# Performance work log

Measured on AMD Instinct MI355X. Metric: run time of the kernel, lower is better.

## Reference

```python
import jax, jax.numpy as jnp
import numpy as np

N_TYPES = 10000   # len(fs.inodes)
HID = 256         # fs.size
BATCH = 32
SEQ = 1024


def _build_tree(rng):
    # random recursive tree: parent[i] uniform in [0, i), root parent = -1
    parent = np.full(N_TYPES, -1, np.int64)
    parent[1:] = (rng.random(N_TYPES - 1) * np.arange(1, N_TYPES)).astype(np.int64)
    # depth (number of nodes on root path incl. self)
    depth = np.ones(N_TYPES, np.int64)
    for i in range(1, N_TYPES):
        depth[i] = depth[parent[i]] + 1
    D = int(depth.max())
    # ancestor table: anc[n, d] = d-th ancestor of n (anc[n,0]=n), -1 padding
    anc = np.full((N_TYPES, D), -1, np.int32)
    anc[:, 0] = np.arange(N_TYPES)
    cur = parent.copy()
    for d in range(1, D):
        anc[:, d] = cur
        cur = np.where(cur >= 0, parent[np.maximum(cur, 0)], -1)
    return anc


def setup_inputs() -> dict:
    key = jax.random.key(0)
    ks = jax.random.split(key, 8)
    rng = np.random.default_rng(0)
    anc = jnp.asarray(_build_tree(rng))  # [N, D] int32
    k = 1.0 / np.sqrt(HID)
    inp = {
        "event_seqs": jax.random.randint(ks[0], (BATCH, SEQ), 0, N_TYPES),
        "anc": anc,
        "weight": jax.random.uniform(ks[1], (N_TYPES,), jnp.float32, -0.1, 0.1),
        "emb": jax.random.normal(ks[2], (N_TYPES, HID), jnp.float32),
        "W_ih": jax.random.uniform(ks[3], (4 * HID, HID), jnp.float32, -k, k),
        "W_hh": jax.random.uniform(ks[4], (4 * HID, HID), jnp.float32, -k, k),
        "b_ih": jax.random.uniform(ks[5], (4 * HID,), jnp.float32, -k, k),
        "b_hh": jax.random.uniform(ks[6], (4 * HID,), jnp.float32, -k, k),
    }
    return inp


def _path_table(anc, weight, emb):
    # path[n] = sum_d (prod_{j<d} weight[anc[n,j]]) * emb[anc[n,d]], over valid ancestors
    valid = anc >= 0                                  # [N, D]
    anc_safe = jnp.where(valid, anc, 0)
    w = jnp.where(valid, weight[anc_safe], 1.0)       # [N, D]
    cumw = jnp.cumprod(w, axis=1)
    cumw = jnp.concatenate([jnp.ones_like(cumw[:, :1]), cumw[:, :-1]], axis=1)
    cumw = jnp.where(valid, cumw, 0.0)
    e = emb[anc_safe]                                 # [N, D, H]
    return jnp.einsum("nd,ndh->nh", cumw, e)          # [N, H]


def _lstm(emb_seq, W_ih, W_hh, b_ih, b_hh):
    # emb_seq: [T, B, H]; torch LSTM gate order i, f, g, o
    H = W_hh.shape[1]
    B = emb_seq.shape[1]
    x_proj = jnp.einsum("tbh,gh->tbg", emb_seq, W_ih) + b_ih + b_hh  # [T, B, 4H]

    def step(carry, x_t):
        h, c = carry
        gates = x_t + h @ W_hh.T
        i, f, g, o = jnp.split(gates, 4, axis=-1)
        i, f, o = jax.nn.sigmoid(i), jax.nn.sigmoid(f), jax.nn.sigmoid(o)
        g = jnp.tanh(g)
        c = f * c + i * g
        h = o * jnp.tanh(c)
        return (h, c), h

    h0 = jnp.zeros((B, H), emb_seq.dtype)
    (hn, cn), out = jax.lax.scan(step, (h0, h0), x_proj)
    return out, hn, cn


def reference(event_seqs, anc, weight, emb, W_ih, W_hh, b_ih, b_hh):
    path = _path_table(anc, weight, emb)       # [N, H]
    emb_seq = path[event_seqs.T]               # [T, B, H] (torch transposes to seq-first)
    out, hn, cn = _lstm(emb_seq, W_ih, W_hh, b_ih, b_hh)
    return out
```

## Files before the change

kernel.cpp:

```cpp
#include <hip/hip_runtime.h>

typedef unsigned int uint;
typedef unsigned long long u64;
typedef _Float16 f16;
typedef _Float16 f16x2 __attribute__((ext_vector_type(2)));
typedef _Float16 f16x8 __attribute__((ext_vector_type(8)));
typedef float f32x4 __attribute__((ext_vector_type(4)));

#define N_TYPES 10000
#define HID 256
#define G4 1024
#define BATCH 32
#define SEQ 1024

__global__ void k_path(const int* __restrict__ anc, const float* __restrict__ weight,
                       const float* __restrict__ emb, int D, f16* __restrict__ path) {
  int n = blockIdx.x;
  int h = threadIdx.x;
  float acc = 0.f, cw = 1.f;
  for (int d = 0; d < D; ++d) {
    int a = anc[n * D + d];
    if (a < 0) break;
    acc += cw * emb[a * HID + h];
    cw *= weight[a];
  }
  path[n * HID + h] = (f16)acc;
}

__global__ void k_conv(const float* __restrict__ wih, const float* __restrict__ whh,
                       const float* __restrict__ bih, const float* __restrict__ bhh,
                       f16* __restrict__ wih_h, uint* __restrict__ whh_t,
                       float* __restrict__ bias) {
  int i = blockIdx.x * 256 + threadIdx.x;
  wih_h[i] = (f16)wih[i];
  if (i < G4 * 128) {
    int row = i >> 7, p = i & 127;
    f16x2 v;
    v.x = (f16)whh[row * HID + 2 * p];
    v.y = (f16)whh[row * HID + 2 * p + 1];
    whh_t[p * G4 + row] = __builtin_bit_cast(uint, v);
  }
  if (i < G4) bias[i] = bih[i] + bhh[i];
}

#define BM 128
#define BN 128
#define BK 64
#define LPAD 72
__global__ __launch_bounds__(256) void k_gemm(const f16* __restrict__ A,
                                              const f16* __restrict__ Bw,
                                              const float* __restrict__ bias,
                                              f16* __restrict__ C) {
  __shared__ f16 sA[BM][LPAD];
  __shared__ f16 sB[BN][LPAD];
  int m0 = blockIdx.x * BM, n0 = blockIdx.y * BN;
  int tid = threadIdx.x;
  int wid = tid >> 6, lane = tid & 63;
  int wm = wid & 1, wn = wid >> 1;
  f32x4 acc[4][4] = {};
  for (int k0 = 0; k0 < 256; k0 += BK) {
    __syncthreads();
    int r = tid >> 3, kc = (tid & 7) * 8;
    for (int i = 0; i < 4; ++i) {
      int row = r + 32 * i;
      int gm = m0 + row;
      uint4 va = make_uint4(0u, 0u, 0u, 0u);
      if (gm < N_TYPES) va = *(const uint4*)&A[gm * 256 + k0 + kc];
      *(uint4*)&sA[row][kc] = va;
      uint4 vb = *(const uint4*)&Bw[(n0 + row) * 256 + k0 + kc];
      *(uint4*)&sB[row][kc] = vb;
    }
    __syncthreads();
#pragma unroll
    for (int ks = 0; ks < 2; ++ks) {
      f16x8 af[4], bf[4];
      int kk = ks * 32 + (lane >> 4) * 8;
#pragma unroll
      for (int mt = 0; mt < 4; ++mt)
        af[mt] = *(const f16x8*)&sA[wm * 64 + mt * 16 + (lane & 15)][kk];
#pragma unroll
      for (int nt = 0; nt < 4; ++nt)
        bf[nt] = *(const f16x8*)&sB[wn * 64 + nt * 16 + (lane & 15)][kk];
#pragma unroll
      for (int mt = 0; mt < 4; ++mt)
#pragma unroll
        for (int nt = 0; nt < 4; ++nt)
          acc[mt][nt] = __builtin_amdgcn_mfma_f32_16x16x32_f16(af[mt], bf[nt], acc[mt][nt], 0, 0, 0);
    }
  }
#pragma unroll
  for (int mt = 0; mt < 4; ++mt)
#pragma unroll
    for (int nt = 0; nt < 4; ++nt)
#pragma unroll
      for (int qq = 0; qq < 4; ++qq) {
        int row = m0 + wm * 64 + mt * 16 + (lane >> 4) * 4 + qq;
        int col = n0 + wn * 64 + nt * 16 + (lane & 15);
        if (row < N_TYPES) C[row * G4 + col] = (f16)(acc[mt][nt][qq] + bias[col]);
      }
}

__device__ __forceinline__ float dot2(uint wp, uint hp, float acc) {
#if __has_builtin(__builtin_amdgcn_fdot2)
  return __builtin_amdgcn_fdot2(__builtin_bit_cast(f16x2, wp),
                                __builtin_bit_cast(f16x2, hp), acc, false);
#else
  f16x2 a = __builtin_bit_cast(f16x2, wp);
  f16x2 b = __builtin_bit_cast(f16x2, hp);
  return acc + (float)a.x * (float)b.x + (float)a.y * (float)b.y;
#endif
}

__device__ __forceinline__ float sigm(float v) { return 1.f / (1.f + __expf(-v)); }
__device__ __forceinline__ float tanh_(float v) { return 1.f - 2.f / (__expf(2.f * v) + 1.f); }

__global__ __launch_bounds__(512, 2)
void k_lstm(const int* __restrict__ evs,
            const f16* __restrict__ proj,
            const uint* __restrict__ whh_t,
            u64* hglob,
            float* __restrict__ out) {
  int bid = blockIdx.x;
  int b = bid & 31, q = bid >> 5;
  int t = threadIdx.x;
  int v = t >> 6, l = t & 63;
  int kq = v >> 1;
  int rid = (v & 1) * 64 + l;
  int rowg = (rid >> 5) * 256 + q * 32 + (rid & 31);

  __shared__ float pl[512];
  __shared__ float rt[128];

  uint w[32];
#pragma unroll
  for (int i = 0; i < 32; ++i) w[i] = whh_t[(kq * 32 + i) * G4 + rowg];

  u64* hb = hglob + b * 256;
  const int* ev = evs + b * SEQ;

  int rrow = (t >> 5) * 256 + q * 32 + (t & 31);
  float x_cur = 0.f, x_nxt = 0.f;
  if (t < 128) x_cur = (float)proj[(long)ev[0] * G4 + rrow];

  float c = 0.f;

  for (int step = 0; step < SEQ; ++step) {
    int h0 = 0;
    if (step > 0) {
      if (l < 32) {
        const u64* src = hb + ((step - 1) & 1) * 128 + kq * 32 + l;
        u64 val;
        do {
          val = __hip_atomic_load(src, __ATOMIC_RELAXED, __HIP_MEMORY_SCOPE_AGENT);
        } while ((uint)(val >> 32) != (uint)step);
        h0 = (int)(uint)val;
      }
    }

    float a0 = 0.f, a1 = 0.f, a2 = 0.f, a3 = 0.f;
#pragma unroll
    for (int i = 0; i < 32; i += 4) {
      a0 = dot2(w[i + 0], (uint)__builtin_amdgcn_readlane(h0, i + 0), a0);
      a1 = dot2(w[i + 1], (uint)__builtin_amdgcn_readlane(h0, i + 1), a1);
      a2 = dot2(w[i + 2], (uint)__builtin_amdgcn_readlane(h0, i + 2), a2);
      a3 = dot2(w[i + 3], (uint)__builtin_amdgcn_readlane(h0, i + 3), a3);
    }
    pl[kq * 128 + rid] = (a0 + a1) + (a2 + a3);

    if (t < 128 && step + 1 < SEQ) x_nxt = (float)proj[(long)ev[step + 1] * G4 + rrow];

    __syncthreads();
    if (t < 128) rt[t] = pl[t] + pl[128 + t] + pl[256 + t] + pl[384 + t] + x_cur;
    __syncthreads();

    if (t < 32) {
      float gi = rt[t], gf = rt[32 + t], gg = rt[64 + t], go = rt[96 + t];
      float iv = sigm(gi), fv = sigm(gf), gv = tanh_(gg), ov = sigm(go);
      c = fv * c + iv * gv;
      float hval = ov * tanh_(c);
      out[(step * BATCH + b) * HID + q * 32 + t] = hval;
      float hA = __shfl(hval, 2 * (t & 15));
      float hB = __shfl(hval, 2 * (t & 15) + 1);
      if (t < 16) {
        f16x2 pk; pk.x = (f16)hA; pk.y = (f16)hB;
        uint pku = __builtin_bit_cast(uint, pk);
        u64 val = (u64)pku | ((u64)(uint)(step + 1) << 32);
        __hip_atomic_store(hb + (step & 1) * 128 + q * 16 + t, val,
                           __ATOMIC_RELAXED, __HIP_MEMORY_SCOPE_AGENT);
      }
    }
    x_cur = x_nxt;
  }
}

extern "C" void kernel_launch(void* const* d_in, const int* in_sizes, int n_in,
                              void* d_out, int out_size, void* d_ws, size_t ws_size,
                              hipStream_t stream) {
  (void)n_in; (void)out_size; (void)ws_size;
  const int* evs = (const int*)d_in[0];
  const int* anc = (const int*)d_in[1];
  const float* weight = (const float*)d_in[2];
  const float* emb = (const float*)d_in[3];
  const float* wih = (const float*)d_in[4];
  const float* whh = (const float*)d_in[5];
  const float* bih = (const float*)d_in[6];
  const float* bhh = (const float*)d_in[7];
  int D = in_sizes[1] / N_TYPES;

  char* ws = (char*)d_ws;
  f16* path = (f16*)(ws);
  f16* wih_h = (f16*)(ws + 5242880);
  uint* whh_t = (uint*)(ws + 5767168);
  float* bias = (float*)(ws + 6291456);
  f16* proj = (f16*)(ws + 6295552);
  u64* hglob = (u64*)(ws + 26775552);
  float* out = (float*)d_out;

  k_conv<<<1024, 256, 0, stream>>>(wih, whh, bih, bhh, wih_h, whh_t, bias);
  k_path<<<N_TYPES, 256, 0, stream>>>(anc, weight, emb, D, path);
  k_gemm<<<dim3(79, 8), 256, 0, stream>>>(path, wih_h, bias, proj);
  hipMemsetAsync(hglob, 0, 32 * 2 * 128 * 8, stream);
  k_lstm<<<256, 512, 0, stream>>>(evs, proj, whh_t, hglob, out);
}
```

Measured before the change: 1.637 ms.

## Reload recurrent weights each step, double-buffer partials, drop second barrier

The LSTM kernel stops keeping its 32 W_hh words in registers and instead reloads them from global memory every step, issued before the spin-wait on h so the loads overlap the wait. The partial-sum buffer is double-buffered so the second __syncthreads can go, and the 32 gate threads now do the four-way reduction themselves using x-projections they fetch directly. This trades register pressure and one barrier per step for extra cached global loads on the serial critical path. The occupancy hint of 2 in the launch bounds is also dropped.

```diff
diff --git a/kernel.cpp b/kernel.cpp
--- a/kernel.cpp
+++ b/kernel.cpp
@@ -114,7 +114,7 @@
 __device__ __forceinline__ float sigm(float v) { return 1.f / (1.f + __expf(-v)); }
 __device__ __forceinline__ float tanh_(float v) { return 1.f - 2.f / (__expf(2.f * v) + 1.f); }
 
-__global__ __launch_bounds__(512, 2)
+__global__ __launch_bounds__(512)
 void k_lstm(const int* __restrict__ evs,
             const f16* __restrict__ proj,
             const uint* __restrict__ whh_t,
@@ -128,23 +128,30 @@
   int rid = (v & 1) * 64 + l;
   int rowg = (rid >> 5) * 256 + q * 32 + (rid & 31);
 
-  __shared__ float pl[512];
-  __shared__ float rt[128];
-
-  uint w[32];
-#pragma unroll
-  for (int i = 0; i < 32; ++i) w[i] = whh_t[(kq * 32 + i) * G4 + rowg];
+  __shared__ float pl[2][512];
 
   u64* hb = hglob + b * 256;
   const int* ev = evs + b * SEQ;
-
-  int rrow = (t >> 5) * 256 + q * 32 + (t & 31);
-  float x_cur = 0.f, x_nxt = 0.f;
-  if (t < 128) x_cur = (float)proj[(long)ev[0] * G4 + rrow];
+  const uint* wbase = whh_t + (kq * 32) * G4 + rowg;
+
+  float x4[4] = {0.f, 0.f, 0.f, 0.f};
+  if (t < 32) {
+    int e0 = ev[0];
+#pragma unroll
+    for (int g = 0; g < 4; ++g)
+      x4[g] = (float)proj[(long)e0 * G4 + g * 256 + q * 32 + t];
+  }
 
   float c = 0.f;
 
   for (int step = 0; step < SEQ; ++step) {
+    uint z = 0;
+    asm volatile("" : "+v"(z));
+    uint wl[32];
+#pragma unroll
+    for (int i = 0; i < 32; ++i) wl[i] = wbase[i * G4 + z];
+    __builtin_amdgcn_sched_barrier(0);
+
     int h0 = 0;
     if (step > 0) {
       if (l < 32) {
@@ -160,22 +167,30 @@
     float a0 = 0.f, a1 = 0.f, a2 = 0.f, a3 = 0.f;
 #pragma unroll
     for (int i = 0; i < 32; i += 4) {
-      a0 = dot2(w[i + 0], (uint)__builtin_amdgcn_readlane(h0, i + 0), a0);
-      a1 = dot2(w[i + 1], (uint)__builtin_amdgcn_readlane(h0, i + 1), a1);
-      a2 = dot2(w[i + 2], (uint)__builtin_amdgcn_readlane(h0, i + 2), a2);
-      a3 = dot2(w[i + 3], (uint)__builtin_amdgcn_readlane(h0, i + 3), a3);
-    }
-    pl[kq * 128 + rid] = (a0 + a1) + (a2 + a3);
-
-    if (t < 128 && step + 1 < SEQ) x_nxt = (float)proj[(long)ev[step + 1] * G4 + rrow];
+      a0 = dot2(wl[i + 0], (uint)__builtin_amdgcn_readlane(h0, i + 0), a0);
+      a1 = dot2(wl[i + 1], (uint)__builtin_amdgcn_readlane(h0, i + 1), a1);
+      a2 = dot2(wl[i + 2], (uint)__builtin_amdgcn_readlane(h0, i + 2), a2);
+      a3 = dot2(wl[i + 3], (uint)__builtin_amdgcn_readlane(h0, i + 3), a3);
+    }
+    pl[step & 1][kq * 128 + rid] = (a0 + a1) + (a2 + a3);
+
+    float x4n[4] = {0.f, 0.f, 0.f, 0.f};
+    if (t < 32 && step + 1 < SEQ) {
+      int e2 = ev[step + 1];
+#pragma unroll
+      for (int g = 0; g < 4; ++g)
+        x4n[g] = (float)proj[(long)e2 * G4 + g * 256 + q * 32 + t];
+    }
 
     __syncthreads();
-    if (t < 128) rt[t] = pl[t] + pl[128 + t] + pl[256 + t] + pl[384 + t] + x_cur;
-    __syncthreads();
 
     if (t < 32) {
-      float gi = rt[t], gf = rt[32 + t], gg = rt[64 + t], go = rt[96 + t];
-      float iv = sigm(gi), fv = sigm(gf), gv = tanh_(gg), ov = sigm(go);
+      const float* pp = pl[step & 1];
+      float s0 = pp[t]        + pp[128 + t]        + pp[256 + t]        + pp[384 + t]        + x4[0];
+      float s1 = pp[32 + t]   + pp[128 + 32 + t]   + pp[256 + 32 + t]   + pp[384 + 32 + t]   + x4[1];
+      float s2 = pp[64 + t]   + pp[128 + 64 + t]   + pp[256 + 64 + t]   + pp[384 + 64 + t]   + x4[2];
+      float s3 = pp[96 + t]   + pp[128 + 96 + t]   + pp[256 + 96 + t]   + pp[384 + 96 + t]   + x4[3];
+      float iv = sigm(s0), fv = sigm(s1), gv = tanh_(s2), ov = sigm(s3);
       c = fv * c + iv * gv;
       float hval = ov * tanh_(c);
       out[(step * BATCH + b) * HID + q * 32 + t] = hval;
@@ -183,13 +198,13 @@
       float hB = __shfl(hval, 2 * (t & 15) + 1);
       if (t < 16) {
         f16x2 pk; pk.x = (f16)hA; pk.y = (f16)hB;
-        uint pku = __builtin_bit_cast(uint, pk);
-        u64 val = (u64)pku | ((u64)(uint)(step + 1) << 32);
+        u64 val = (u64)__builtin_bit_cast(uint, pk) | ((u64)(uint)(step + 1) << 32);
         __hip_atomic_store(hb + (step & 1) * 128 + q * 16 + t, val,
                            __ATOMIC_RELAXED, __HIP_MEMORY_SCOPE_AGENT);
       }
     }
-    x_cur = x_nxt;
+#pragma unroll
+    for (int g = 0; g < 4; ++g) x4[g] = x4n[g];
   }
 }
 
```

After: 1.999 ms. 22.1% more time.

## Drop second LSTM barrier via double-buffered partials and gate-interleaved projection layout

Applied to the files above, without the earlier changes.

The GEMM output is now stored with the four gates of each hidden unit interleaved, so one thread fetches all four input-projection gates with a single 8-byte load. Per-step partial sums go into a double-buffered shared array, which lets the gate threads reduce them directly after one barrier instead of two. Recurrent weights move from registers into 64 KB of LDS and are reread every step, and the launch bound no longer asks for two blocks per CU. The aim is to shorten the serial per-step critical path, at the cost of extra LDS traffic in the dot-product loop.

```diff
diff --git a/kernel.cpp b/kernel.cpp
--- a/kernel.cpp
+++ b/kernel.cpp
@@ -2,6 +2,7 @@
 
 typedef unsigned int uint;
 typedef unsigned long long u64;
+typedef unsigned short ushort;
 typedef _Float16 f16;
 typedef _Float16 f16x2 __attribute__((ext_vector_type(2)));
 typedef _Float16 f16x8 __attribute__((ext_vector_type(8)));
@@ -96,7 +97,9 @@
       for (int qq = 0; qq < 4; ++qq) {
         int row = m0 + wm * 64 + mt * 16 + (lane >> 4) * 4 + qq;
         int col = n0 + wn * 64 + nt * 16 + (lane & 15);
-        if (row < N_TYPES) C[row * G4 + col] = (f16)(acc[mt][nt][qq] + bias[col]);
+        int dim = col & 255, g = col >> 8;
+        if (row < N_TYPES)
+          C[row * G4 + dim * 4 + g] = (f16)(acc[mt][nt][qq] + bias[col]);
       }
 }
 
@@ -113,8 +116,9 @@
 
 __device__ __forceinline__ float sigm(float v) { return 1.f / (1.f + __expf(-v)); }
 __device__ __forceinline__ float tanh_(float v) { return 1.f - 2.f / (__expf(2.f * v) + 1.f); }
-
-__global__ __launch_bounds__(512, 2)
+__device__ __forceinline__ float f16u(ushort u) { return (float)__builtin_bit_cast(f16, u); }
+
+__global__ __launch_bounds__(512)
 void k_lstm(const int* __restrict__ evs,
             const f16* __restrict__ proj,
             const uint* __restrict__ whh_t,
@@ -128,54 +132,74 @@
   int rid = (v & 1) * 64 + l;
   int rowg = (rid >> 5) * 256 + q * 32 + (rid & 31);
 
-  __shared__ float pl[512];
-  __shared__ float rt[128];
-
-  uint w[32];
-#pragma unroll
-  for (int i = 0; i < 32; ++i) w[i] = whh_t[(kq * 32 + i) * G4 + rowg];
+  __shared__ uint4 wlds[8 * 512];
+  __shared__ float pl[2][128][4];
+
+  {
+    const uint* wb = whh_t + (kq * 32) * G4 + rowg;
+#pragma unroll
+    for (int i4 = 0; i4 < 8; ++i4) {
+      uint4 wv;
+      wv.x = wb[(4 * i4 + 0) * G4];
+      wv.y = wb[(4 * i4 + 1) * G4];
+      wv.z = wb[(4 * i4 + 2) * G4];
+      wv.w = wb[(4 * i4 + 3) * G4];
+      wlds[i4 * 512 + t] = wv;
+    }
+  }
+  __syncthreads();
 
   u64* hb = hglob + b * 256;
   const int* ev = evs + b * SEQ;
 
-  int rrow = (t >> 5) * 256 + q * 32 + (t & 31);
-  float x_cur = 0.f, x_nxt = 0.f;
-  if (t < 128) x_cur = (float)proj[(long)ev[0] * G4 + rrow];
+  float x0 = 0.f, x1 = 0.f, x2 = 0.f, x3 = 0.f;
+  if (t < 32) {
+    ushort4 xv = *(const ushort4*)(proj + (long)ev[0] * G4 + (q * 32 + t) * 4);
+    x0 = f16u(xv.x); x1 = f16u(xv.y); x2 = f16u(xv.z); x3 = f16u(xv.w);
+  }
 
   float c = 0.f;
 
   for (int step = 0; step < SEQ; ++step) {
     int h0 = 0;
-    if (step > 0) {
-      if (l < 32) {
-        const u64* src = hb + ((step - 1) & 1) * 128 + kq * 32 + l;
-        u64 val;
-        do {
-          val = __hip_atomic_load(src, __ATOMIC_RELAXED, __HIP_MEMORY_SCOPE_AGENT);
-        } while ((uint)(val >> 32) != (uint)step);
-        h0 = (int)(uint)val;
-      }
+    if (step > 0 && l < 32) {
+      const u64* src = hb + ((step - 1) & 1) * 128 + kq * 32 + l;
+      u64 val;
+      do {
+        val = __hip_atomic_load(src, __ATOMIC_RELAXED, __HIP_MEMORY_SCOPE_AGENT);
+      } while ((uint)(val >> 32) != (uint)step);
+      h0 = (int)(uint)val;
     }
 
     float a0 = 0.f, a1 = 0.f, a2 = 0.f, a3 = 0.f;
 #pragma unroll
-    for (int i = 0; i < 32; i += 4) {
-      a0 = dot2(w[i + 0], (uint)__builtin_amdgcn_readlane(h0, i + 0), a0);
-      a1 = dot2(w[i + 1], (uint)__builtin_amdgcn_readlane(h0, i + 1), a1);
-      a2 = dot2(w[i + 2], (uint)__builtin_amdgcn_readlane(h0, i + 2), a2);
-      a3 = dot2(w[i + 3], (uint)__builtin_amdgcn_readlane(h0, i + 3), a3);
-    }
-    pl[kq * 128 + rid] = (a0 + a1) + (a2 + a3);
-
-    if (t < 128 && step + 1 < SEQ) x_nxt = (float)proj[(long)ev[step + 1] * G4 + rrow];
+    for (int i4 = 0; i4 < 8; ++i4) {
+      uint4 wv = wlds[i4 * 512 + t];
+      a0 = dot2(wv.x, (uint)__builtin_amdgcn_readlane(h0, 4 * i4 + 0), a0);
+      a1 = dot2(wv.y, (uint)__builtin_amdgcn_readlane(h0, 4 * i4 + 1), a1);
+      a2 = dot2(wv.z, (uint)__builtin_amdgcn_readlane(h0, 4 * i4 + 2), a2);
+      a3 = dot2(wv.w, (uint)__builtin_amdgcn_readlane(h0, 4 * i4 + 3), a3);
+    }
+    pl[step & 1][rid][kq] = (a0 + a1) + (a2 + a3);
+
+    float n0 = 0.f, n1 = 0.f, n2 = 0.f, n3 = 0.f;
+    if (t < 32 && step + 1 < SEQ) {
+      ushort4 xv = *(const ushort4*)(proj + (long)ev[step + 1] * G4 + (q * 32 + t) * 4);
+      n0 = f16u(xv.x); n1 = f16u(xv.y); n2 = f16u(xv.z); n3 = f16u(xv.w);
+    }
 
     __syncthreads();
-    if (t < 128) rt[t] = pl[t] + pl[128 + t] + pl[256 + t] + pl[384 + t] + x_cur;
-    __syncthreads();
 
     if (t < 32) {
-      float gi = rt[t], gf = rt[32 + t], gg = rt[64 + t], go = rt[96 + t];
-      float iv = sigm(gi), fv = sigm(gf), gv = tanh_(gg), ov = sigm(go);
+      f32x4 p0 = *(const f32x4*)&pl[step & 1][t][0];
+      f32x4 p1 = *(const f32x4*)&pl[step & 1][32 + t][0];
+      f32x4 p2 = *(const f32x4*)&pl[step & 1][64 + t][0];
+      f32x4 p3 = *(const f32x4*)&pl[step & 1][96 + t][0];
+      float s0 = (p0[0] + p0[1]) + (p0[2] + p0[3]) + x0;
+      float s1 = (p1[0] + p1[1]) + (p1[2] + p1[3]) + x1;
+      float s2 = (p2[0] + p2[1]) + (p2[2] + p2[3]) + x2;
+      float s3 = (p3[0] + p3[1]) + (p3[2] + p3[3]) + x3;
+      float iv = sigm(s0), fv = sigm(s1), gv = tanh_(s2), ov = sigm(s3);
       c = fv * c + iv * gv;
       float hval = ov * tanh_(c);
       out[(step * BATCH + b) * HID + q * 32 + t] = hval;
@@ -183,13 +207,12 @@
       float hB = __shfl(hval, 2 * (t & 15) + 1);
       if (t < 16) {
         f16x2 pk; pk.x = (f16)hA; pk.y = (f16)hB;
-        uint pku = __builtin_bit_cast(uint, pk);
-        u64 val = (u64)pku | ((u64)(uint)(step + 1) << 32);
+        u64 val = (u64)__builtin_bit_cast(uint, pk) | ((u64)(uint)(step + 1) << 32);
         __hip_atomic_store(hb + (step & 1) * 128 + q * 16 + t, val,
                            __ATOMIC_RELAXED, __HIP_MEMORY_SCOPE_AGENT);
       }
     }
-    x_cur = x_nxt;
+    x0 = n0; x1 = n1; x2 = n2; x3 = n3;
   }
 }
 
```

Result: slower. 1.815 ms (+10.9%).

## Interleave gate projections, drop a barrier with double-buffered partials in LSTM

Applied to the files above, without the earlier changes.

The GEMM epilogue now stores the projection gate-interleaved per hidden dimension, so each of the 32 finishing threads loads its four gate inputs with one 8-byte load. The per-step second __syncthreads and the rt staging buffer are removed. Partial sums are double-buffered by step parity so the 32 finishing threads reduce the four k-slices directly. The h publish now happens before the output store and next-x prefetch, and the polling moves to the upper half-wave lanes, both aiming to shorten the serial critical path per timestep. The prefetch is now serialized inside the 32-lane tail, which may expose its latency instead of hiding it.

```diff
diff --git a/kernel.cpp b/kernel.cpp
--- a/kernel.cpp
+++ b/kernel.cpp
@@ -2,6 +2,7 @@
 
 typedef unsigned int uint;
 typedef unsigned long long u64;
+typedef unsigned short ushort;
 typedef _Float16 f16;
 typedef _Float16 f16x2 __attribute__((ext_vector_type(2)));
 typedef _Float16 f16x8 __attribute__((ext_vector_type(8)));
@@ -96,7 +97,9 @@
       for (int qq = 0; qq < 4; ++qq) {
         int row = m0 + wm * 64 + mt * 16 + (lane >> 4) * 4 + qq;
         int col = n0 + wn * 64 + nt * 16 + (lane & 15);
-        if (row < N_TYPES) C[row * G4 + col] = (f16)(acc[mt][nt][qq] + bias[col]);
+        int dim = col & 255, g = col >> 8;
+        if (row < N_TYPES)
+          C[row * G4 + dim * 4 + g] = (f16)(acc[mt][nt][qq] + bias[col]);
       }
 }
 
@@ -113,6 +116,7 @@
 
 __device__ __forceinline__ float sigm(float v) { return 1.f / (1.f + __expf(-v)); }
 __device__ __forceinline__ float tanh_(float v) { return 1.f - 2.f / (__expf(2.f * v) + 1.f); }
+__device__ __forceinline__ float f16u(ushort u) { return (float)__builtin_bit_cast(f16, u); }
 
 __global__ __launch_bounds__(512, 2)
 void k_lstm(const int* __restrict__ evs,
@@ -128,8 +132,7 @@
   int rid = (v & 1) * 64 + l;
   int rowg = (rid >> 5) * 256 + q * 32 + (rid & 31);
 
-  __shared__ float pl[512];
-  __shared__ float rt[128];
+  __shared__ float pl[2][4][128];
 
   uint w[32];
 #pragma unroll
@@ -138,47 +141,46 @@
   u64* hb = hglob + b * 256;
   const int* ev = evs + b * SEQ;
 
-  int rrow = (t >> 5) * 256 + q * 32 + (t & 31);
-  float x_cur = 0.f, x_nxt = 0.f;
-  if (t < 128) x_cur = (float)proj[(long)ev[0] * G4 + rrow];
+  float x0 = 0.f, x1 = 0.f, x2 = 0.f, x3 = 0.f;
+  if (t < 32) {
+    ushort4 xv = *(const ushort4*)(proj + (long)ev[0] * G4 + (q * 32 + t) * 4);
+    x0 = f16u(xv.x); x1 = f16u(xv.y); x2 = f16u(xv.z); x3 = f16u(xv.w);
+  }
 
   float c = 0.f;
 
   for (int step = 0; step < SEQ; ++step) {
     int h0 = 0;
-    if (step > 0) {
-      if (l < 32) {
-        const u64* src = hb + ((step - 1) & 1) * 128 + kq * 32 + l;
-        u64 val;
-        do {
-          val = __hip_atomic_load(src, __ATOMIC_RELAXED, __HIP_MEMORY_SCOPE_AGENT);
-        } while ((uint)(val >> 32) != (uint)step);
-        h0 = (int)(uint)val;
-      }
+    if (step > 0 && l >= 32) {
+      const u64* src = hb + ((step - 1) & 1) * 128 + kq * 32 + (l - 32);
+      u64 val;
+      do {
+        val = __hip_atomic_load(src, __ATOMIC_RELAXED, __HIP_MEMORY_SCOPE_AGENT);
+      } while ((uint)(val >> 32) != (uint)step);
+      h0 = (int)(uint)val;
     }
 
     float a0 = 0.f, a1 = 0.f, a2 = 0.f, a3 = 0.f;
 #pragma unroll
     for (int i = 0; i < 32; i += 4) {
-      a0 = dot2(w[i + 0], (uint)__builtin_amdgcn_readlane(h0, i + 0), a0);
-      a1 = dot2(w[i + 1], (uint)__builtin_amdgcn_readlane(h0, i + 1), a1);
-      a2 = dot2(w[i + 2], (uint)__builtin_amdgcn_readlane(h0, i + 2), a2);
-      a3 = dot2(w[i + 3], (uint)__builtin_amdgcn_readlane(h0, i + 3), a3);
-    }
-    pl[kq * 128 + rid] = (a0 + a1) + (a2 + a3);
-
-    if (t < 128 && step + 1 < SEQ) x_nxt = (float)proj[(long)ev[step + 1] * G4 + rrow];
+      a0 = dot2(w[i + 0], (uint)__builtin_amdgcn_readlane(h0, 32 + i + 0), a0);
+      a1 = dot2(w[i + 1], (uint)__builtin_amdgcn_readlane(h0, 32 + i + 1), a1);
+      a2 = dot2(w[i + 2], (uint)__builtin_amdgcn_readlane(h0, 32 + i + 2), a2);
+      a3 = dot2(w[i + 3], (uint)__builtin_amdgcn_readlane(h0, 32 + i + 3), a3);
+    }
+    pl[step & 1][kq][rid] = (a0 + a1) + (a2 + a3);
 
     __syncthreads();
-    if (t < 128) rt[t] = pl[t] + pl[128 + t] + pl[256 + t] + pl[384 + t] + x_cur;
-    __syncthreads();
 
     if (t < 32) {
-      float gi = rt[t], gf = rt[32 + t], gg = rt[64 + t], go = rt[96 + t];
-      float iv = sigm(gi), fv = sigm(gf), gv = tanh_(gg), ov = sigm(go);
+      const float (*pp)[128] = pl[step & 1];
+      float s0 = (pp[0][t]      + pp[1][t])      + (pp[2][t]      + pp[3][t])      + x0;
+      float s1 = (pp[0][32 + t] + pp[1][32 + t]) + (pp[2][32 + t] + pp[3][32 + t]) + x1;
+      float s2 = (pp[0][64 + t] + pp[1][64 + t]) + (pp[2][64 + t] + pp[3][64 + t]) + x2;
+      float s3 = (pp[0][96 + t] + pp[1][96 + t]) + (pp[2][96 + t] + pp[3][96 + t]) + x3;
+      float iv = sigm(s0), fv = sigm(s1), gv = tanh_(s2), ov = sigm(s3);
       c = fv * c + iv * gv;
       float hval = ov * tanh_(c);
-      out[(step * BATCH + b) * HID + q * 32 + t] = hval;
       float hA = __shfl(hval, 2 * (t & 15));
       float hB = __shfl(hval, 2 * (t & 15) + 1);
       if (t < 16) {
@@ -188,8 +190,12 @@
         __hip_atomic_store(hb + (step & 1) * 128 + q * 16 + t, val,
                            __ATOMIC_RELAXED, __HIP_MEMORY_SCOPE_AGENT);
       }
-    }
-    x_cur = x_nxt;
+      out[(step * BATCH + b) * HID + q * 32 + t] = hval;
+      if (step + 1 < SEQ) {
+        ushort4 xv = *(const ushort4*)(proj + (long)ev[step + 1] * G4 + (q * 32 + t) * 4);
+        x0 = f16u(xv.x); x1 = f16u(xv.y); x2 = f16u(xv.z); x3 = f16u(xv.w);
+      }
+    }
   }
 }
 
```

Result: no change. 1.633 ms (-0.2%).
